# Kernel optimization log

Measured on AMD Instinct MI355X. Metric: run time of the kernel, lower is better.

The kernel has to match this reference:

```python
import jax, jax.numpy as jnp
import numpy as np


def _pyramid(x2, k):
    # AdaptiveAvgPool2d(k) with H,W divisible by k == block mean, then nearest upsample back
    B, C, H, W = x2.shape
    p = x2.reshape(B, C, k, H // k, k, W // k).mean(axis=(3, 5))  # [B,C,k,k]
    return jnp.repeat(jnp.repeat(p, H // k, axis=2), W // k, axis=3)  # [B,C,H,W]


def setup_inputs() -> dict:
    key = jax.random.key(0)
    ks = jax.random.split(key, 8)
    B, C, H, W = 32, 256, 32, 32
    x1 = jax.random.normal(ks[0], (B, C, H, W), jnp.float32)
    x2 = jax.random.normal(ks[1], (B, C, H, W), jnp.float32)
    # 1x1 conv weights (kaiming-ish scale), stored as [out,in]
    Wq = jax.random.normal(ks[2], (C // 2, C), jnp.float32) * (1.0 / np.sqrt(C))
    bq = jnp.zeros((C // 2,), jnp.float32)
    Wk = jax.random.normal(ks[3], (C // 2, 4 * C), jnp.float32) * (1.0 / np.sqrt(4 * C))
    bk = jnp.zeros((C // 2,), jnp.float32)
    Wv = jax.random.normal(ks[4], (C, C), jnp.float32) * (1.0 / np.sqrt(C))
    bv = jnp.zeros((C,), jnp.float32)
    return {"x1": x1, "x2": x2, "Wq": Wq, "bq": bq, "Wk": Wk, "bk": bk, "Wv": Wv, "bv": bv}


def reference(x1, x2, Wq, bq, Wk, bk, Wv, bv):
    B, C, H, W = x1.shape
    HW = H * W
    # pyramid pool at scales 1,2,4, upsampled and concatenated with x2 -> [B,4C,H,W]
    x2p = jnp.concatenate([x2] + [_pyramid(x2, k) for k in (1, 2, 4)], axis=1)
    # 1x1 convs as channel contractions
    q = (jnp.einsum('oc,bchw->bohw', Wq, x1) + bq[None, :, None, None]).reshape(B, C // 2, HW)
    k = (jnp.einsum('oc,bchw->bohw', Wk, x2p) + bk[None, :, None, None]).reshape(B, C // 2, HW)
    v = (jnp.einsum('oc,bchw->bohw', Wv, x2) + bv[None, :, None, None]).reshape(B, C, HW)
    query = q.transpose(0, 2, 1)                         # [B,HW,C/2]
    attn = jax.nn.softmax(jnp.einsum('bic,bcj->bij', query, k), axis=-1)  # [B,HW,HW]
    out = jnp.einsum('bcj,bij->bci', v, attn).reshape(B, C, H, W)
    return out + x1
```

## Files before the change

### kernel.cpp

```cpp
#include <hip/hip_runtime.h>


typedef __attribute__((ext_vector_type(8))) short short8;
typedef __attribute__((ext_vector_type(4))) float f32x4;

#define MFMA(a, b, c) __builtin_amdgcn_mfma_f32_16x16x32_bf16((a), (b), (c), 0, 0, 0)

#define GLOAD16(gp, lp)                                                        \
    __builtin_amdgcn_global_load_lds(                                          \
        (const __attribute__((address_space(1))) unsigned int*)(gp),           \
        (__attribute__((address_space(3))) unsigned int*)(lp), 16, 0, 0)

__device__ __forceinline__ unsigned short f2bf(float f) {
    unsigned u = __builtin_bit_cast(unsigned, f);
    u = (u + 0x7FFFu + ((u >> 16) & 1u)) >> 16;
    return (unsigned short)u;
}
__device__ __forceinline__ short8 ld8(const unsigned short* p) {
    return *reinterpret_cast<const short8*>(p);
}
__device__ __forceinline__ short8 ld8b(const void* base, int byte_off) {
    return *reinterpret_cast<const short8*>((const char*)base + byte_off);
}

__global__ __launch_bounds__(64) void pool_kernel(const float* __restrict__ x2,
                                                  float* __restrict__ p1,
                                                  float* __restrict__ p2,
                                                  float* __restrict__ p4) {
    int bc = blockIdx.x;
    int t = threadIdx.x;
    const float* src = x2 + (size_t)bc * 1024;
    int dh = t >> 3, dw = t & 7;
    float s[16];
#pragma unroll
    for (int r = 0; r < 16; ++r)
        s[r] = src[((r >> 2) * 8 + dh) * 32 + (r & 3) * 8 + dw];
#pragma unroll
    for (int r = 0; r < 16; ++r) {
        float v = s[r];
        v += __shfl_xor(v, 1);  v += __shfl_xor(v, 2);  v += __shfl_xor(v, 4);
        v += __shfl_xor(v, 8);  v += __shfl_xor(v, 16); v += __shfl_xor(v, 32);
        s[r] = v;
    }
    if (t == 0) {
        float sq[4];
#pragma unroll
        for (int j = 0; j < 4; ++j) {
            int jh = j >> 1, jw = j & 1;
            sq[j] = s[8 * jh + 2 * jw] + s[8 * jh + 2 * jw + 1] +
                    s[8 * jh + 4 + 2 * jw] + s[8 * jh + 4 + 2 * jw + 1];
            p2[(size_t)bc * 4 + j] = sq[j] * (1.f / 256.f);
        }
#pragma unroll
        for (int r = 0; r < 16; ++r) p4[(size_t)bc * 16 + r] = s[r] * (1.f / 64.f);
        p1[bc] = (sq[0] + sq[1] + sq[2] + sq[3]) * (1.f / 1024.f);
    }
}

__global__ __launch_bounds__(256) void kadd_kernel(const float* __restrict__ Wk,
                                                   const float* __restrict__ bk,
                                                   const float* __restrict__ p1,
                                                   const float* __restrict__ p2,
                                                   const float* __restrict__ p4,
                                                   float* __restrict__ kadd) {
    int b = blockIdx.x >> 7, o = blockIdx.x & 127;
    int tid = threadIdx.x;
    const float* wr = Wk + (size_t)o * 1024;
    int c = tid;
    size_t bc = (size_t)b * 256 + c;
    float vals[21];
    vals[0] = wr[256 + c] * p1[bc];
    float w2 = wr[512 + c], w4 = wr[768 + c];
#pragma unroll
    for (int j = 0; j < 4; ++j) vals[1 + j] = w2 * p2[bc * 4 + j];
#pragma unroll
    for (int r = 0; r < 16; ++r) vals[5 + r] = w4 * p4[bc * 16 + r];

    int lane = tid & 63, wid = tid >> 6;
    __shared__ float red[21][4];
    __shared__ float tot[21];
#pragma unroll
    for (int k = 0; k < 21; ++k) {
        float v = vals[k];
        v += __shfl_xor(v, 1);  v += __shfl_xor(v, 2);  v += __shfl_xor(v, 4);
        v += __shfl_xor(v, 8);  v += __shfl_xor(v, 16); v += __shfl_xor(v, 32);
        if (lane == 0) red[k][wid] = v;
    }
    __syncthreads();
    if (tid < 21) tot[tid] = red[tid][0] + red[tid][1] + red[tid][2] + red[tid][3];
    __syncthreads();
    if (tid < 16) {
        int r = tid;
        int rr = ((r >> 2) >> 1) * 2 + ((r & 3) >> 1);
        kadd[((size_t)(b * 128 + o)) * 16 + r] = bk[o] + tot[0] + tot[1 + rr] + tot[5 + r];
    }
}

__device__ __forceinline__ void stage_x(unsigned short* lds, const float* X,
                                        int n0, int kc, int tid) {
    int c4 = (tid & 15) * 4;
    int ng = tid >> 4;
    const float* src = X + (size_t)(kc + c4) * 1024 + n0 + ng * 8;
    float v[4][8];
#pragma unroll
    for (int i = 0; i < 4; ++i) {
        f32x4 a = *reinterpret_cast<const f32x4*>(src + (size_t)i * 1024);
        f32x4 bb = *reinterpret_cast<const f32x4*>(src + (size_t)i * 1024 + 4);
#pragma unroll
        for (int t = 0; t < 4; ++t) { v[i][t] = a[t]; v[i][4 + t] = bb[t]; }
    }
#pragma unroll
    for (int j = 0; j < 8; ++j) {
        int n = ng * 8 + j;
        uint2 pk;
        pk.x = (unsigned)f2bf(v[0][j]) | ((unsigned)f2bf(v[1][j]) << 16);
        pk.y = (unsigned)f2bf(v[2][j]) | ((unsigned)f2bf(v[3][j]) << 16);
        int byte = (n << 7) + (((tid & 15) * 8) ^ ((n & 7) << 4));
        *reinterpret_cast<uint2*>((char*)lds + byte) = pk;
    }
}
__device__ __forceinline__ void stage_w(unsigned short* lds, const float* W, int ldw,
                                        int o0, int kc, int tid) {
    int o = tid >> 1, h = tid & 1;
    const float* src = W + (size_t)(o0 + o) * ldw + kc + h * 32;
    float v[32];
#pragma unroll
    for (int q = 0; q < 8; ++q) {
        f32x4 a = *reinterpret_cast<const f32x4*>(src + q * 4);
#pragma unroll
        for (int t = 0; t < 4; ++t) v[q * 4 + t] = a[t];
    }
    int swz = (o & 7) << 4;
#pragma unroll
    for (int q = 0; q < 4; ++q) {
        uint4 pk;
        pk.x = (unsigned)f2bf(v[q*8+0]) | ((unsigned)f2bf(v[q*8+1]) << 16);
        pk.y = (unsigned)f2bf(v[q*8+2]) | ((unsigned)f2bf(v[q*8+3]) << 16);
        pk.z = (unsigned)f2bf(v[q*8+4]) | ((unsigned)f2bf(v[q*8+5]) << 16);
        pk.w = (unsigned)f2bf(v[q*8+6]) | ((unsigned)f2bf(v[q*8+7]) << 16);
        int byte = (o << 7) + (((h * 64) + q * 16) ^ swz);
        *reinterpret_cast<uint4*>((char*)lds + byte) = pk;
    }
}

__global__ __launch_bounds__(256) void gemm_kernel(const float* __restrict__ x1,
                                                   const float* __restrict__ x2,
                                                   const float* __restrict__ Wq,
                                                   const float* __restrict__ bq,
                                                   const float* __restrict__ Wk,
                                                   const float* __restrict__ Wv,
                                                   const float* __restrict__ bv,
                                                   const float* __restrict__ kadd,
                                                   unsigned short* __restrict__ qt,
                                                   unsigned short* __restrict__ kt,
                                                   unsigned short* __restrict__ vv) {
    __shared__ unsigned short alds[128 * 64];
    __shared__ unsigned short blds[128 * 64];

    int id = blockIdx.x;
    int mode, bx, by = 0, b;
    if (id < 256)      { mode = 0; b = id >> 3; bx = id & 7; }
    else if (id < 512) { mode = 1; b = (id - 256) >> 3; bx = (id - 256) & 7; }
    else               { int t = id - 512; mode = 2; b = t >> 4; bx = (t >> 3) & 1; by = t & 7; }

    int tid = threadIdx.x;
    int w = tid >> 6, lane = tid & 63;
    int lrow = lane & 15, lk16b = (lane >> 4) * 16;
    int swl = (lrow & 7) << 4;
    int row0 = bx * 128;
    int col0 = (mode == 2) ? by * 128 : 0;
    int wr = (w >> 1) * 64, wc = (w & 1) * 64;

    const float* X = ((mode == 0) ? x1 : x2) + (size_t)b * 262144;
    const float* Wmat = (mode == 0) ? Wq : (mode == 1) ? Wk : Wv;
    int ldw = (mode == 1) ? 1024 : 256;

    f32x4 z = {0.f, 0.f, 0.f, 0.f};
    f32x4 acc[4][4];
#pragma unroll
    for (int i = 0; i < 4; ++i)
#pragma unroll
        for (int j = 0; j < 4; ++j) acc[i][j] = z;

    for (int kc = 0; kc < 256; kc += 64) {
        if (kc) __syncthreads();
        if (mode != 2) {
            stage_x(alds, X, row0, kc, tid);
            stage_w(blds, Wmat, ldw, 0, kc, tid);
        } else {
            stage_w(alds, Wmat, ldw, row0, kc, tid);
            stage_x(blds, X, col0, kc, tid);
        }
        __syncthreads();

#pragma unroll
        for (int kh = 0; kh < 2; ++kh) {
            short8 af[4], bfr[4];
#pragma unroll
            for (int i = 0; i < 4; ++i)
                af[i] = ld8b(alds, ((wr + i * 16 + lrow) << 7) + (((kh << 6) + lk16b) ^ swl));
#pragma unroll
            for (int j = 0; j < 4; ++j)
                bfr[j] = ld8b(blds, ((wc + j * 16 + lrow) << 7) + (((kh << 6) + lk16b) ^ swl));
#pragma unroll
            for (int i = 0; i < 4; ++i)
#pragma unroll
                for (int j = 0; j < 4; ++j) acc[i][j] = MFMA(af[i], bfr[j], acc[i][j]);
        }
    }

    unsigned short* out = (mode == 0) ? qt + (size_t)b * 131072
                        : (mode == 1) ? kt + (size_t)b * 131072
                                      : vv + (size_t)b * 262144;
    int ldo = (mode == 2) ? 1024 : 128;
#pragma unroll
    for (int i = 0; i < 4; ++i) {
#pragma unroll
        for (int j = 0; j < 4; ++j) {
            int col = col0 + wc + j * 16 + lrow;
#pragma unroll
            for (int r = 0; r < 4; ++r) {
                int row = row0 + wr + i * 16 + (lane >> 4) * 4 + r;
                float val = acc[i][j][r];
                if (mode == 0) val += bq[col];
                if (mode == 1) {
                    int h = row >> 5, ww = row & 31;
                    val += kadd[((size_t)(b * 128 + col)) * 16 + ((h >> 3) * 4 + (ww >> 3))];
                }
                if (mode == 2) val += bv[row];
                out[(size_t)row * ldo + col] = f2bf(val);
            }
        }
    }
}

__global__ __launch_bounds__(256) void attn_kernel(const unsigned short* __restrict__ qt,
                                                   const unsigned short* __restrict__ kt,
                                                   const unsigned short* __restrict__ vv,
                                                   const float* __restrict__ x1,
                                                   float* __restrict__ out) {
    int bid = blockIdx.x;
    int lid = bid >> 3;
    int b = (bid & 7) * 4 + (lid >> 4);
    int i0 = (lid & 15) * 64;
    int tid = threadIdx.x;
    int w = tid >> 6, lane = tid & 63;
    int lrow = lane & 15, lk8 = (lane >> 4) * 8;
    int lk16b = lk8 * 2;
    int swl = (lrow & 7) << 4;
    int iw = i0 + w * 16;

    __shared__ unsigned short klds[2][64 * 128];
    __shared__ unsigned short vlds[256 * 64];
    __shared__ unsigned short plds[4][16][72];

    const unsigned short* qb = qt + ((size_t)b * 1024 + iw) * 128;
    const unsigned short* kb = kt + (size_t)b * 131072;
    const unsigned short* vb = vv + (size_t)b * 262144;

    short8 qf[4];
#pragma unroll
    for (int cc = 0; cc < 4; ++cc) qf[cc] = ld8(qb + (size_t)lrow * 128 + cc * 32 + lk8);

    int soff = w * 1024 + (lane << 4);
    int krow0 = soff >> 8;
    int kcol = ((soff & 255) ^ ((krow0 & 7) << 4)) >> 1;
    int vrow0 = soff >> 7;
    int vcol = ((soff & 127) ^ ((vrow0 & 7) << 4)) >> 1;

    f32x4 z = {0.f, 0.f, 0.f, 0.f};
    f32x4 oacc[16];
#pragma unroll
    for (int cb = 0; cb < 16; ++cb) oacc[cb] = z;
    float m_[4] = {-1e30f, -1e30f, -1e30f, -1e30f};
    float l_[4] = {0.f, 0.f, 0.f, 0.f};

#pragma unroll
    for (int it = 0; it < 4; ++it)
        GLOAD16(kb + (size_t)(it * 16 + krow0) * 128 + kcol,
                (char*)klds + it * 4096 + w * 1024);

    int cur = 0;
    for (int j0 = 0; j0 < 1024; j0 += 64) {
        asm volatile("s_waitcnt vmcnt(0)" ::: "memory");
        __syncthreads();

#pragma unroll
        for (int it = 0; it < 8; ++it)
            GLOAD16(vb + (size_t)(it * 32 + vrow0) * 1024 + j0 + vcol,
                    (char*)vlds + it * 4096 + w * 1024);

        const char* kbase = (const char*)klds + cur * 16384;
        f32x4 s[4];
#pragma unroll
        for (int jb = 0; jb < 4; ++jb) s[jb] = z;
#pragma unroll
        for (int jb = 0; jb < 4; ++jb) {
            int jrow = jb * 16 + lrow;
#pragma unroll
            for (int cc = 0; cc < 4; ++cc) {
                short8 kf = ld8b(kbase, (jrow << 8) + (((cc << 6) + lk16b) ^ swl));
                s[jb] = MFMA(qf[cc], kf, s[jb]);
            }
        }

        int jn = (j0 + 64) & 1023;
#pragma unroll
        for (int it = 0; it < 4; ++it)
            GLOAD16(kb + (size_t)(jn + it * 16 + krow0) * 128 + kcol,
                    (char*)klds + (cur ^ 1) * 16384 + it * 4096 + w * 1024);

        float tmax[4];
#pragma unroll
        for (int r = 0; r < 4; ++r) {
            float t = fmaxf(fmaxf(s[0][r], s[1][r]), fmaxf(s[2][r], s[3][r]));
            t = fmaxf(t, __shfl_xor(t, 1));
            t = fmaxf(t, __shfl_xor(t, 2));
            t = fmaxf(t, __shfl_xor(t, 4));
            t = fmaxf(t, __shfl_xor(t, 8));
            tmax[r] = t;
        }
        bool ok = (tmax[0] <= m_[0] + 8.f) && (tmax[1] <= m_[1] + 8.f) &&
                  (tmax[2] <= m_[2] + 8.f) && (tmax[3] <= m_[3] + 8.f);
        if (!__all(ok)) {
#pragma unroll
            for (int r = 0; r < 4; ++r) {
                float nm = fmaxf(m_[r], tmax[r]);
                float sc = __expf(m_[r] - nm);
                m_[r] = nm;
                l_[r] *= sc;
#pragma unroll
                for (int cb = 0; cb < 16; ++cb) oacc[cb][r] *= sc;
            }
        }
        float rs[4] = {0.f, 0.f, 0.f, 0.f};
#pragma unroll
        for (int jb = 0; jb < 4; ++jb)
#pragma unroll
            for (int r = 0; r < 4; ++r) {
                float p = __expf(s[jb][r] - m_[r]);
                rs[r] += p;
                plds[w][(lane >> 4) * 4 + r][jb * 16 + lrow] = f2bf(p);
            }
#pragma unroll
        for (int r = 0; r < 4; ++r) {
            float t = rs[r];
            t += __shfl_xor(t, 1);
            t += __shfl_xor(t, 2);
            t += __shfl_xor(t, 4);
            t += __shfl_xor(t, 8);
            l_[r] += t;
        }

        asm volatile("s_waitcnt vmcnt(4)" ::: "memory");
        __syncthreads();

        short8 pa0 = ld8(&plds[w][lrow][lk8]);
        short8 pa1 = ld8(&plds[w][lrow][32 + lk8]);
#pragma unroll
        for (int cb = 0; cb < 16; ++cb) {
            int c = cb * 16 + lrow;
            short8 vf0 = ld8b(vlds, (c << 7) + (lk16b ^ swl));
            oacc[cb] = MFMA(pa0, vf0, oacc[cb]);
            short8 vf1 = ld8b(vlds, (c << 7) + ((64 + lk16b) ^ swl));
            oacc[cb] = MFMA(pa1, vf1, oacc[cb]);
        }
        cur ^= 1;
    }
    asm volatile("s_waitcnt vmcnt(0)" ::: "memory");

    float inv[4];
#pragma unroll
    for (int r = 0; r < 4; ++r) inv[r] = 1.f / l_[r];
    int ib = iw + (lane >> 4) * 4;
#pragma unroll
    for (int cb = 0; cb < 16; ++cb) {
        int c = cb * 16 + lrow;
        size_t g = ((size_t)b * 256 + c) * 1024 + ib;
        f32x4 xv = *reinterpret_cast<const f32x4*>(x1 + g);
        f32x4 res;
#pragma unroll
        for (int r = 0; r < 4; ++r) res[r] = oacc[cb][r] * inv[r] + xv[r];
        *reinterpret_cast<f32x4*>(out + g) = res;
    }
}

extern "C" void kernel_launch(void* const* d_in, const int* in_sizes, int n_in,
                              void* d_out, int out_size, void* d_ws, size_t ws_size,
                              hipStream_t stream) {
    const float* x1 = (const float*)d_in[0];
    const float* x2 = (const float*)d_in[1];
    const float* Wq = (const float*)d_in[2];
    const float* bq = (const float*)d_in[3];
    const float* Wk = (const float*)d_in[4];
    const float* bk = (const float*)d_in[5];
    const float* Wv = (const float*)d_in[6];
    const float* bv = (const float*)d_in[7];
    float* out = (float*)d_out;

    char* ws = (char*)d_ws;
    unsigned short* qt = (unsigned short*)(ws + 0);
    unsigned short* kt = (unsigned short*)(ws + 8388608);
    unsigned short* v  = (unsigned short*)(ws + 16777216);
    float* p1   = (float*)(ws + 33554432);
    float* p2   = (float*)(ws + 33587200);
    float* p4   = (float*)(ws + 33718272);
    float* kadd = (float*)(ws + 34242560);

    pool_kernel<<<8192, 64, 0, stream>>>(x2, p1, p2, p4);
    kadd_kernel<<<4096, 256, 0, stream>>>(Wk, bk, p1, p2, p4, kadd);
    gemm_kernel<<<1024, 256, 0, stream>>>(x1, x2, Wq, bq, Wk, Wv, bv, kadd, qt, kt, v);
    attn_kernel<<<512, 256, 0, stream>>>(qt, kt, v, x1, out);
}
```

Before: 261.3 us.

## Prefetch next X tile in projection GEMM, use packed bf16 convert, widen pool blocks

The projection GEMM now issues the global loads for the next K-chunk of the activation tile into registers before the MFMA loop of the current chunk, so memory latency overlaps compute instead of stalling right after each barrier. The float-to-bf16 packing uses the hardware v_cvt_pk_bf16_f32 instruction instead of manual rounding arithmetic. The pool kernel packs four (b,c) planes per 256-thread block instead of one per 64-thread block. The prefetch adds 32 live float registers per thread, which may reduce occupancy.

```diff
diff --git a/kernel.cpp b/kernel.cpp
--- a/kernel.cpp
+++ b/kernel.cpp
@@ -16,6 +16,11 @@
     u = (u + 0x7FFFu + ((u >> 16) & 1u)) >> 16;
     return (unsigned short)u;
 }
+__device__ __forceinline__ unsigned cvt_pk(float lo, float hi) {
+    unsigned r;
+    asm("v_cvt_pk_bf16_f32 %0, %1, %2" : "=v"(r) : "v"(lo), "v"(hi));
+    return r;
+}
 __device__ __forceinline__ short8 ld8(const unsigned short* p) {
     return *reinterpret_cast<const short8*>(p);
 }
@@ -23,12 +28,12 @@
     return *reinterpret_cast<const short8*>((const char*)base + byte_off);
 }
 
-__global__ __launch_bounds__(64) void pool_kernel(const float* __restrict__ x2,
-                                                  float* __restrict__ p1,
-                                                  float* __restrict__ p2,
-                                                  float* __restrict__ p4) {
-    int bc = blockIdx.x;
-    int t = threadIdx.x;
+__global__ __launch_bounds__(256) void pool_kernel(const float* __restrict__ x2,
+                                                   float* __restrict__ p1,
+                                                   float* __restrict__ p2,
+                                                   float* __restrict__ p4) {
+    int w = threadIdx.x >> 6, t = threadIdx.x & 63;
+    int bc = blockIdx.x * 4 + w;
     const float* src = x2 + (size_t)bc * 1024;
     int dh = t >> 3, dw = t & 7;
     float s[16];
@@ -96,50 +101,50 @@
     }
 }
 
-__device__ __forceinline__ void stage_x(unsigned short* lds, const float* X,
-                                        int n0, int kc, int tid) {
-    int c4 = (tid & 15) * 4;
-    int ng = tid >> 4;
+__device__ __forceinline__ void ldx(const float* X, int n0, int kc, int tid,
+                                    float v[32]) {
+    int c4 = (tid & 15) * 4, ng = tid >> 4;
     const float* src = X + (size_t)(kc + c4) * 1024 + n0 + ng * 8;
-    float v[4][8];
 #pragma unroll
     for (int i = 0; i < 4; ++i) {
         f32x4 a = *reinterpret_cast<const f32x4*>(src + (size_t)i * 1024);
-        f32x4 bb = *reinterpret_cast<const f32x4*>(src + (size_t)i * 1024 + 4);
-#pragma unroll
-        for (int t = 0; t < 4; ++t) { v[i][t] = a[t]; v[i][4 + t] = bb[t]; }
-    }
+        f32x4 b = *reinterpret_cast<const f32x4*>(src + (size_t)i * 1024 + 4);
+#pragma unroll
+        for (int t = 0; t < 4; ++t) { v[i * 8 + t] = a[t]; v[i * 8 + 4 + t] = b[t]; }
+    }
+}
+__device__ __forceinline__ void packx(unsigned short* lds, int tid, const float v[32]) {
+    int c8b = (tid & 15) * 8, ng = tid >> 4;
 #pragma unroll
     for (int j = 0; j < 8; ++j) {
         int n = ng * 8 + j;
         uint2 pk;
-        pk.x = (unsigned)f2bf(v[0][j]) | ((unsigned)f2bf(v[1][j]) << 16);
-        pk.y = (unsigned)f2bf(v[2][j]) | ((unsigned)f2bf(v[3][j]) << 16);
-        int byte = (n << 7) + (((tid & 15) * 8) ^ ((n & 7) << 4));
-        *reinterpret_cast<uint2*>((char*)lds + byte) = pk;
-    }
-}
-__device__ __forceinline__ void stage_w(unsigned short* lds, const float* W, int ldw,
-                                        int o0, int kc, int tid) {
+        pk.x = cvt_pk(v[0 * 8 + j], v[1 * 8 + j]);
+        pk.y = cvt_pk(v[2 * 8 + j], v[3 * 8 + j]);
+        *reinterpret_cast<uint2*>((char*)lds + (n << 7) + (c8b ^ ((n & 7) << 4))) = pk;
+    }
+}
+__device__ __forceinline__ void ldw_tile(const float* W, int ldW, int o0, int kc,
+                                         int tid, float v[32]) {
     int o = tid >> 1, h = tid & 1;
-    const float* src = W + (size_t)(o0 + o) * ldw + kc + h * 32;
-    float v[32];
+    const float* src = W + (size_t)(o0 + o) * ldW + kc + h * 32;
 #pragma unroll
     for (int q = 0; q < 8; ++q) {
         f32x4 a = *reinterpret_cast<const f32x4*>(src + q * 4);
 #pragma unroll
         for (int t = 0; t < 4; ++t) v[q * 4 + t] = a[t];
     }
-    int swz = (o & 7) << 4;
+}
+__device__ __forceinline__ void packw(unsigned short* lds, int tid, const float v[32]) {
+    int o = tid >> 1, h = tid & 1, swz = (o & 7) << 4;
 #pragma unroll
     for (int q = 0; q < 4; ++q) {
         uint4 pk;
-        pk.x = (unsigned)f2bf(v[q*8+0]) | ((unsigned)f2bf(v[q*8+1]) << 16);
-        pk.y = (unsigned)f2bf(v[q*8+2]) | ((unsigned)f2bf(v[q*8+3]) << 16);
-        pk.z = (unsigned)f2bf(v[q*8+4]) | ((unsigned)f2bf(v[q*8+5]) << 16);
-        pk.w = (unsigned)f2bf(v[q*8+6]) | ((unsigned)f2bf(v[q*8+7]) << 16);
-        int byte = (o << 7) + (((h * 64) + q * 16) ^ swz);
-        *reinterpret_cast<uint4*>((char*)lds + byte) = pk;
+        pk.x = cvt_pk(v[q * 8 + 0], v[q * 8 + 1]);
+        pk.y = cvt_pk(v[q * 8 + 2], v[q * 8 + 3]);
+        pk.z = cvt_pk(v[q * 8 + 4], v[q * 8 + 5]);
+        pk.w = cvt_pk(v[q * 8 + 6], v[q * 8 + 7]);
+        *reinterpret_cast<uint4*>((char*)lds + (o << 7) + (((h * 64) + q * 16) ^ swz)) = pk;
     }
 }
 
@@ -173,7 +178,11 @@
 
     const float* X = ((mode == 0) ? x1 : x2) + (size_t)b * 262144;
     const float* Wmat = (mode == 0) ? Wq : (mode == 1) ? Wk : Wv;
-    int ldw = (mode == 1) ? 1024 : 256;
+    int ldW = (mode == 1) ? 1024 : 256;
+    int xbase = (mode == 2) ? col0 : row0;
+    int wbase = (mode == 2) ? row0 : 0;
+    unsigned short* xl = (mode == 2) ? blds : alds;
+    unsigned short* wl = (mode == 2) ? alds : blds;
 
     f32x4 z = {0.f, 0.f, 0.f, 0.f};
     f32x4 acc[4][4];
@@ -182,15 +191,15 @@
 #pragma unroll
         for (int j = 0; j < 4; ++j) acc[i][j] = z;
 
+    float xv[32], wv[32];
+    ldx(X, xbase, 0, tid, xv);
+
     for (int kc = 0; kc < 256; kc += 64) {
+        ldw_tile(Wmat, ldW, wbase, kc, tid, wv);
         if (kc) __syncthreads();
-        if (mode != 2) {
-            stage_x(alds, X, row0, kc, tid);
-            stage_w(blds, Wmat, ldw, 0, kc, tid);
-        } else {
-            stage_w(alds, Wmat, ldw, row0, kc, tid);
-            stage_x(blds, X, col0, kc, tid);
-        }
+        packx(xl, tid, xv);
+        packw(wl, tid, wv);
+        if (kc < 192) ldx(X, xbase, kc + 64, tid, xv);
         __syncthreads();
 
 #pragma unroll
@@ -407,7 +416,7 @@
     float* p4   = (float*)(ws + 33718272);
     float* kadd = (float*)(ws + 34242560);
 
-    pool_kernel<<<8192, 64, 0, stream>>>(x2, p1, p2, p4);
+    pool_kernel<<<2048, 256, 0, stream>>>(x2, p1, p2, p4);
     kadd_kernel<<<4096, 256, 0, stream>>>(Wk, bk, p1, p2, p4, kadd);
     gemm_kernel<<<1024, 256, 0, stream>>>(x1, x2, Wq, bq, Wk, Wv, bv, kadd, qt, kt, v);
     attn_kernel<<<512, 256, 0, stream>>>(qt, kt, v, x1, out);
```

After: 259.1 us. About the same (-0.8%).
